# Performance work log

Measured on AMD Instinct MI355X. Metric: run time of the kernel, lower is better.

The kernel has to match this reference:

```python
import jax, jax.numpy as jnp
import numpy as np

NUM_CLASSES = 256  # all classes present in ys -> unique(ys) == arange(NUM_CLASSES)
T = 1.0
MIN_SAMPLES = 3


def setup_inputs() -> dict:
    key = jax.random.key(0)
    k1, k2, k3, k4, k5 = jax.random.split(key, 5)
    xq = jax.random.normal(k1, (512, 512), dtype=jnp.float32)
    yq = jax.random.randint(k2, (512,), 0, NUM_CLASSES)
    xs = jax.random.normal(k3, (8192, 512), dtype=jnp.float32)
    ys = jax.random.randint(k4, (8192,), 0, NUM_CLASSES)
    pos = jax.random.randint(k5, (512,), 0, 8192)
    return {"xq": xq, "yq": yq, "xs": xs, "ys": ys, "pos": pos}


def _intra_class_variance_l2(x, y, num_classes):
    # vectorized version of compute_intra_class_variance(..., distance='l2_dist')
    ones = jnp.ones(y.shape[0], x.dtype)
    counts = jax.ops.segment_sum(ones, y, num_segments=num_classes)          # [C]
    sums = jax.ops.segment_sum(x, y, num_segments=num_classes)               # [C,D]
    means = sums / jnp.maximum(counts, 1.0)[:, None]
    d2 = jnp.sum((x - means[y]) ** 2, axis=-1)                               # [N]
    var_c = jax.ops.segment_sum(d2, y, num_segments=num_classes) / jnp.maximum(counts, 1.0)
    valid = counts >= MIN_SAMPLES
    tot = jnp.sum(jnp.where(valid, var_c * counts, 0.0))
    cnt = jnp.sum(jnp.where(valid, counts, 0.0))
    return jnp.where(cnt > 0, tot / jnp.maximum(cnt, 1.0), 0.0)


def reference(xq, yq, xs, ys, pos):
    B = xq.shape[0]
    # classes = unique(ys) == arange(NUM_CLASSES); one_hot[pos].nonzero()[:,1] == ys[pos]
    yq_new = ys[pos]                                                          # [B]

    var_intra = _intra_class_variance_l2(xq, yq, NUM_CLASSES)                 # no-grad diagnostic

    ones = jnp.ones(ys.shape[0], xq.dtype)
    class_count = jax.ops.segment_sum(ones, ys, num_segments=NUM_CLASSES)    # [C]
    mus = jax.ops.segment_sum(xs, ys, num_segments=NUM_CLASSES)              # [C,D] class-sum prototypes

    idx = jnp.arange(B)
    # leave-one-out corrections
    M = jnp.broadcast_to(mus[None], (B,) + mus.shape).at[idx, yq_new].add(-xq)          # [B,C,D]
    Cn = jnp.broadcast_to(class_count[None], (B, NUM_CLASSES)).at[idx, yq_new].add(-1.0)  # [B,C]

    proto = M / jnp.maximum(Cn, 0.1)[..., None]
    logit = -0.5 * jnp.sum((xq[:, None, :] - proto) ** 2, axis=-1)            # [B,C] (l2_dist)
    logit = logit * (Cn > 0.1)

    logp = jax.nn.log_softmax(logit / T, axis=-1)
    loss = -jnp.mean(jnp.take_along_axis(logp, yq_new[:, None], axis=1))
    return (loss, var_intra)
```

## Files before the change

### kernel.cpp

```cpp
#include <hip/hip_runtime.h>

#define D 512
#define C 256
#define B 512
#define NS 8192

__device__ __forceinline__ float wave_sum(float v) {
#pragma unroll
    for (int off = 32; off > 0; off >>= 1) v += __shfl_xor(v, off, 64);
    return v;
}
__device__ __forceinline__ float wave_max(float v) {
#pragma unroll
    for (int off = 32; off > 0; off >>= 1) v = fmaxf(v, __shfl_xor(v, off, 64));
    return v;
}
__device__ __forceinline__ float block_sum8(float v, float* sm) {
    v = wave_sum(v);
    int tid = threadIdx.x;
    if ((tid & 63) == 0) sm[tid >> 6] = v;
    __syncthreads();
    float r = ((sm[0] + sm[1]) + (sm[2] + sm[3])) + ((sm[4] + sm[5]) + (sm[6] + sm[7]));
    __syncthreads();
    return r;
}
__device__ __forceinline__ float half_sum(float v, float* sm) {
    v = wave_sum(v);
    int tid = threadIdx.x;
    if ((tid & 63) == 0) sm[tid >> 6] = v;
    __syncthreads();
    int base = (tid >> 8) << 2;
    float r = (sm[base] + sm[base + 1]) + (sm[base + 2] + sm[base + 3]);
    __syncthreads();
    return r;
}
__device__ __forceinline__ float half_max(float v, float* sm) {
    v = wave_max(v);
    int tid = threadIdx.x;
    if ((tid & 63) == 0) sm[tid >> 6] = v;
    __syncthreads();
    int base = (tid >> 8) << 2;
    float r = fmaxf(fmaxf(sm[base], sm[base + 1]), fmaxf(sm[base + 2], sm[base + 3]));
    __syncthreads();
    return r;
}

__global__ void stats_kernel(const float* __restrict__ xq, const int* __restrict__ yq,
                             const float* __restrict__ xs, const int* __restrict__ ys,
                             float* __restrict__ musT, float* __restrict__ counts,
                             float* __restrict__ nm, float* __restrict__ qcount,
                             float* __restrict__ d2sum, float* __restrict__ nq,
                             float* __restrict__ out) {
    __shared__ int list[NS];
    __shared__ int cnt;
    __shared__ float sm[8];
    int bid = blockIdx.x, tid = threadIdx.x;

    if (bid < C) {
        int c = bid;
        if (tid == 0) cnt = 0;
        __syncthreads();
        for (int i = tid; i < NS; i += 512)
            if (ys[i] == c) { int p = atomicAdd(&cnt, 1); list[p] = i; }
        __syncthreads();
        int n = cnt;
        float acc[16];
#pragma unroll
        for (int k = 0; k < 16; ++k) acc[k] = 0.f;
        for (int base = 0; base < n; base += 16) {
#pragma unroll
            for (int k = 0; k < 16; ++k) {
                int jj = base + k;
                int row = list[jj < n ? jj : n - 1];
                float v = xs[(size_t)row * D + tid];
                acc[k] += (jj < n) ? v : 0.f;
            }
        }
        float m = (((acc[0] + acc[1]) + (acc[2] + acc[3])) + ((acc[4] + acc[5]) + (acc[6] + acc[7]))) +
                  (((acc[8] + acc[9]) + (acc[10] + acc[11])) + ((acc[12] + acc[13]) + (acc[14] + acc[15])));
        if (n == 0) m = 0.f;
        musT[(size_t)tid * C + c] = m;
        float s = block_sum8(m * m, sm);
        if (tid == 0) { nm[c] = s; counts[c] = (float)n; }
    } else {
        int c = bid - C;
        if (tid == 0) cnt = 0;
        __syncthreads();
        if (yq[tid] == c) { int p = atomicAdd(&cnt, 1); list[p] = tid; }
        __syncthreads();
        int n = cnt;
        float ssum = 0.f, tsq = 0.f;
        for (int j = 0; j < n; ++j) {
            int row = list[j];
            float v = xq[(size_t)row * D + tid];
            ssum += v;
            float rq = block_sum8(v * v, sm);
            if (tid == 0) nq[row] = rq;
            tsq += rq;
        }
        float nrm = block_sum8(ssum * ssum, sm);
        if (tid == 0) {
            qcount[c] = (float)n;
            d2sum[c] = (n > 0) ? (tsq - nrm / (float)n) : 0.f;
            if (c == 0) out[0] = 0.f;
        }
    }
}

__global__ void loss_kernel(const float* __restrict__ xq, const int* __restrict__ ys,
                            const int* __restrict__ pos, const float* __restrict__ musT,
                            const float* __restrict__ nm, const float* __restrict__ cc,
                            const float* __restrict__ nq, const float* __restrict__ qcount,
                            const float* __restrict__ d2sum, float* __restrict__ out) {
    __shared__ float part[2][8][C];
    __shared__ float sm[8];
    __shared__ float sh_t[2];
    int tid = threadIdx.x;
    int b0 = blockIdx.x * 2;
    int lane = tid & 63;
    int ks = tid >> 6;
    int dbase = ks << 6;
    int cbase = lane << 2;

    float xr0 = xq[(size_t)(b0 + 0) * D + dbase + lane];
    float xr1 = xq[(size_t)(b0 + 1) * D + dbase + lane];

    const float* mtb = musT + (size_t)dbase * C + cbase;
    float4 a0 = make_float4(0.f, 0.f, 0.f, 0.f);
    float4 a1 = make_float4(0.f, 0.f, 0.f, 0.f);
#pragma unroll
    for (int j0 = 0; j0 < 64; j0 += 8) {
        float4 m[8];
#pragma unroll
        for (int k = 0; k < 8; ++k)
            m[k] = *(const float4*)(mtb + (size_t)(j0 + k) * C);
#pragma unroll
        for (int k = 0; k < 8; ++k) {
            float x0 = __int_as_float(__builtin_amdgcn_readlane(__float_as_int(xr0), j0 + k));
            float x1 = __int_as_float(__builtin_amdgcn_readlane(__float_as_int(xr1), j0 + k));
            a0.x += m[k].x * x0; a0.y += m[k].y * x0; a0.z += m[k].z * x0; a0.w += m[k].w * x0;
            a1.x += m[k].x * x1; a1.y += m[k].y * x1; a1.z += m[k].z * x1; a1.w += m[k].w * x1;
        }
    }
    *(float4*)&part[0][ks][cbase] = a0;
    *(float4*)&part[1][ks][cbase] = a1;
    __syncthreads();

    int h = tid >> 8;
    int c = tid & (C - 1);
    int b = b0 + h;
    float g = 0.f;
#pragma unroll
    for (int k = 0; k < 8; ++k) g += part[h][k][c];

    int t = ys[pos[b]];
    float nqv = nq[b];
    float count = cc[c], nmv = nm[c];
    float Cn = count, dt = g, m2 = nmv;
    if (c == t) { Cn -= 1.0f; dt = g - nqv; m2 = nmv - 2.0f * g + nqv; }
    float den = fmaxf(Cn, 0.1f);
    float inv = 1.0f / den;
    float dist2 = nqv - 2.0f * dt * inv + m2 * inv * inv;
    float logit = (Cn > 0.1f) ? (-0.5f * dist2) : 0.0f;
    if (c == t) sh_t[h] = logit;

    float mx = half_max(logit, sm);
    float e = expf(logit - mx);
    float se = half_sum(e, sm);
    if (c == 0) atomicAdd(out, -(sh_t[h] - mx - logf(se)) * (1.0f / (float)B));

    if (blockIdx.x == 0) {
        float cv = (tid < C) ? qcount[tid] : 0.f;
        float dv = (tid < C) ? d2sum[tid] : 0.f;
        bool valid = cv >= 3.0f;
        float tot = block_sum8(valid ? dv : 0.f, sm);
        float ctot = block_sum8(valid ? cv : 0.f, sm);
        if (tid == 0) out[1] = (ctot > 0.f) ? tot / fmaxf(ctot, 1.0f) : 0.0f;
    }
}

extern "C" void kernel_launch(void* const* d_in, const int* in_sizes, int n_in,
                              void* d_out, int out_size, void* d_ws, size_t ws_size,
                              hipStream_t stream) {
    const float* xq = (const float*)d_in[0];
    const int* yq = (const int*)d_in[1];
    const float* xs = (const float*)d_in[2];
    const int* ys = (const int*)d_in[3];
    const int* pos = (const int*)d_in[4];
    float* out = (float*)d_out;

    float* ws = (float*)d_ws;
    float* musT = ws;
    float* counts = ws + 131072;
    float* nm = ws + 131328;
    float* qcount = ws + 131584;
    float* d2sum = ws + 131840;
    float* nq = ws + 132096;

    stats_kernel<<<2 * C, 512, 0, stream>>>(xq, yq, xs, ys, musT, counts, nm,
                                            qcount, d2sum, nq, out);
    loss_kernel<<<C, 512, 0, stream>>>(xq, ys, pos, musT, nm, counts, nq,
                                       qcount, d2sum, out);
}
```

Before: 26.39 us.

## Store class-sum prototypes as bf16 and restructure gather, norm and query-stat reductions

Class-sum prototypes are now written as bf16 (round-to-nearest-even) and unpacked in the loss kernel, halving the musT traffic between the two kernels. The gather in the stats kernel changes from scalar per-thread loads to float4 loads with four row groups, combined through shared memory. Query squared norms are recomputed inside the loss kernel instead of being stored, and the per-row block reductions in the query-stats branch become one final reduction. bf16 prototypes add rounding error to the logits and the loss, which may break tolerance.

```diff
diff --git a/kernel.cpp b/kernel.cpp
--- a/kernel.cpp
+++ b/kernel.cpp
@@ -45,15 +45,16 @@
     return r;
 }
 
-__global__ void stats_kernel(const float* __restrict__ xq, const int* __restrict__ yq,
-                             const float* __restrict__ xs, const int* __restrict__ ys,
-                             float* __restrict__ musT, float* __restrict__ counts,
-                             float* __restrict__ nm, float* __restrict__ qcount,
-                             float* __restrict__ d2sum, float* __restrict__ nq,
-                             float* __restrict__ out) {
-    __shared__ int list[NS];
+__global__ __launch_bounds__(512) void stats_kernel(
+        const float* __restrict__ xq, const int* __restrict__ yq,
+        const float* __restrict__ xs, const int* __restrict__ ys,
+        unsigned short* __restrict__ musT, float* __restrict__ counts,
+        float* __restrict__ nm, float* __restrict__ qcount,
+        float* __restrict__ d2sum, float* __restrict__ out) {
+    __shared__ unsigned short list[NS];
     __shared__ int cnt;
     __shared__ float sm[8];
+    __shared__ __align__(16) float part4[4][D];
     int bid = blockIdx.x, tid = threadIdx.x;
 
     if (bid < C) {
@@ -61,44 +62,54 @@
         if (tid == 0) cnt = 0;
         __syncthreads();
         for (int i = tid; i < NS; i += 512)
-            if (ys[i] == c) { int p = atomicAdd(&cnt, 1); list[p] = i; }
+            if (ys[i] == c) { int p = atomicAdd(&cnt, 1); list[p] = (unsigned short)i; }
         __syncthreads();
         int n = cnt;
-        float acc[16];
-#pragma unroll
-        for (int k = 0; k < 16; ++k) acc[k] = 0.f;
-        for (int base = 0; base < n; base += 16) {
-#pragma unroll
-            for (int k = 0; k < 16; ++k) {
-                int jj = base + k;
-                int row = list[jj < n ? jj : n - 1];
-                float v = xs[(size_t)row * D + tid];
-                acc[k] += (jj < n) ? v : 0.f;
+        int q = tid >> 7, l = tid & 127;
+        float4 acc = make_float4(0.f, 0.f, 0.f, 0.f);
+        for (int base = 0; base < n; base += 32) {
+            float4 mv[8];
+            float w[8];
+#pragma unroll
+            for (int k = 0; k < 8; ++k) {
+                int jj = base + (k << 2) + q;
+                int cj = jj < n ? jj : n - 1;
+                int row = list[cj];
+                mv[k] = *(const float4*)(xs + (size_t)row * D + (l << 2));
+                w[k] = (jj < n) ? 1.f : 0.f;
             }
-        }
-        float m = (((acc[0] + acc[1]) + (acc[2] + acc[3])) + ((acc[4] + acc[5]) + (acc[6] + acc[7]))) +
-                  (((acc[8] + acc[9]) + (acc[10] + acc[11])) + ((acc[12] + acc[13]) + (acc[14] + acc[15])));
-        if (n == 0) m = 0.f;
-        musT[(size_t)tid * C + c] = m;
+#pragma unroll
+            for (int k = 0; k < 8; ++k) {
+                acc.x = fmaf(mv[k].x, w[k], acc.x);
+                acc.y = fmaf(mv[k].y, w[k], acc.y);
+                acc.z = fmaf(mv[k].z, w[k], acc.z);
+                acc.w = fmaf(mv[k].w, w[k], acc.w);
+            }
+        }
+        *(float4*)&part4[q][l << 2] = acc;
+        __syncthreads();
+        float m = (part4[0][tid] + part4[1][tid]) + (part4[2][tid] + part4[3][tid]);
+        unsigned int u = __float_as_uint(m);
+        u += 0x7fffu + ((u >> 16) & 1u);
+        musT[(size_t)tid * C + c] = (unsigned short)(u >> 16);
         float s = block_sum8(m * m, sm);
         if (tid == 0) { nm[c] = s; counts[c] = (float)n; }
     } else {
         int c = bid - C;
         if (tid == 0) cnt = 0;
         __syncthreads();
-        if (yq[tid] == c) { int p = atomicAdd(&cnt, 1); list[p] = tid; }
+        if (yq[tid] == c) { int p = atomicAdd(&cnt, 1); list[p] = (unsigned short)tid; }
         __syncthreads();
         int n = cnt;
-        float ssum = 0.f, tsq = 0.f;
+        float ssum = 0.f, sq = 0.f;
         for (int j = 0; j < n; ++j) {
             int row = list[j];
             float v = xq[(size_t)row * D + tid];
             ssum += v;
-            float rq = block_sum8(v * v, sm);
-            if (tid == 0) nq[row] = rq;
-            tsq += rq;
+            sq = fmaf(v, v, sq);
         }
         float nrm = block_sum8(ssum * ssum, sm);
+        float tsq = block_sum8(sq, sm);
         if (tid == 0) {
             qcount[c] = (float)n;
             d2sum[c] = (n > 0) ? (tsq - nrm / (float)n) : 0.f;
@@ -107,11 +118,12 @@
     }
 }
 
-__global__ void loss_kernel(const float* __restrict__ xq, const int* __restrict__ ys,
-                            const int* __restrict__ pos, const float* __restrict__ musT,
-                            const float* __restrict__ nm, const float* __restrict__ cc,
-                            const float* __restrict__ nq, const float* __restrict__ qcount,
-                            const float* __restrict__ d2sum, float* __restrict__ out) {
+__global__ __launch_bounds__(512) void loss_kernel(
+        const float* __restrict__ xq, const int* __restrict__ ys,
+        const int* __restrict__ pos, const unsigned short* __restrict__ musT,
+        const float* __restrict__ nm, const float* __restrict__ cc,
+        const float* __restrict__ qcount, const float* __restrict__ d2sum,
+        float* __restrict__ out) {
     __shared__ float part[2][8][C];
     __shared__ float sm[8];
     __shared__ float sh_t[2];
@@ -124,22 +136,30 @@
 
     float xr0 = xq[(size_t)(b0 + 0) * D + dbase + lane];
     float xr1 = xq[(size_t)(b0 + 1) * D + dbase + lane];
-
-    const float* mtb = musT + (size_t)dbase * C + cbase;
+    float nq0 = block_sum8(xr0 * xr0, sm);
+    float nq1 = block_sum8(xr1 * xr1, sm);
+
+    const unsigned short* mtb = musT + (size_t)dbase * C + cbase;
     float4 a0 = make_float4(0.f, 0.f, 0.f, 0.f);
     float4 a1 = make_float4(0.f, 0.f, 0.f, 0.f);
 #pragma unroll
     for (int j0 = 0; j0 < 64; j0 += 8) {
-        float4 m[8];
+        uint2 mv[8];
 #pragma unroll
         for (int k = 0; k < 8; ++k)
-            m[k] = *(const float4*)(mtb + (size_t)(j0 + k) * C);
+            mv[k] = *(const uint2*)(mtb + (size_t)(j0 + k) * C);
 #pragma unroll
         for (int k = 0; k < 8; ++k) {
             float x0 = __int_as_float(__builtin_amdgcn_readlane(__float_as_int(xr0), j0 + k));
             float x1 = __int_as_float(__builtin_amdgcn_readlane(__float_as_int(xr1), j0 + k));
-            a0.x += m[k].x * x0; a0.y += m[k].y * x0; a0.z += m[k].z * x0; a0.w += m[k].w * x0;
-            a1.x += m[k].x * x1; a1.y += m[k].y * x1; a1.z += m[k].z * x1; a1.w += m[k].w * x1;
+            float c0 = __uint_as_float(mv[k].x << 16);
+            float c1 = __uint_as_float(mv[k].x & 0xffff0000u);
+            float c2 = __uint_as_float(mv[k].y << 16);
+            float c3 = __uint_as_float(mv[k].y & 0xffff0000u);
+            a0.x = fmaf(c0, x0, a0.x); a0.y = fmaf(c1, x0, a0.y);
+            a0.z = fmaf(c2, x0, a0.z); a0.w = fmaf(c3, x0, a0.w);
+            a1.x = fmaf(c0, x1, a1.x); a1.y = fmaf(c1, x1, a1.y);
+            a1.z = fmaf(c2, x1, a1.z); a1.w = fmaf(c3, x1, a1.w);
         }
     }
     *(float4*)&part[0][ks][cbase] = a0;
@@ -154,7 +174,7 @@
     for (int k = 0; k < 8; ++k) g += part[h][k][c];
 
     int t = ys[pos[b]];
-    float nqv = nq[b];
+    float nqv = h ? nq1 : nq0;
     float count = cc[c], nmv = nm[c];
     float Cn = count, dt = g, m2 = nmv;
     if (c == t) { Cn -= 1.0f; dt = g - nqv; m2 = nmv - 2.0f * g + nqv; }
@@ -189,16 +209,15 @@
     const int* pos = (const int*)d_in[4];
     float* out = (float*)d_out;
 
-    float* ws = (float*)d_ws;
-    float* musT = ws;
-    float* counts = ws + 131072;
-    float* nm = ws + 131328;
-    float* qcount = ws + 131584;
-    float* d2sum = ws + 131840;
-    float* nq = ws + 132096;
+    float* wsf = (float*)d_ws;
+    unsigned short* musT = (unsigned short*)d_ws;
+    float* counts = wsf + 65536;
+    float* nm = wsf + 65792;
+    float* qcount = wsf + 66048;
+    float* d2sum = wsf + 66304;
 
     stats_kernel<<<2 * C, 512, 0, stream>>>(xq, yq, xs, ys, musT, counts, nm,
-                                            qcount, d2sum, nq, out);
-    loss_kernel<<<C, 512, 0, stream>>>(xq, ys, pos, musT, nm, counts, nq,
+                                            qcount, d2sum, out);
+    loss_kernel<<<C, 512, 0, stream>>>(xq, ys, pos, musT, nm, counts,
                                        qcount, d2sum, out);
 }
```

Result: faster. 25.00 us (-5.3%).
